# Performance work log

Hardware: AMD Instinct MI355X
Metric: run time of the kernel (lower is better)

Reference implementation:

```python
import jax, jax.numpy as jnp
import numpy as np
import math

NEG = -1e9
B, TX, TY, ODIM = 32, 512, 2048, 80


def setup_inputs() -> dict:
    key = jax.random.key(0)
    k1, k2 = jax.random.split(key)
    return {
        "x_m": jax.random.normal(k1, (B, TX, ODIM), jnp.float32),
        "x_logs": jnp.zeros((B, TX, ODIM), jnp.float32),  # mean_only=True -> zeros_like(x_m)
        "z": jax.random.normal(k2, (B, ODIM, TY), jnp.float32),
        "x_mask": jnp.ones((B, 1, TX), jnp.float32),
        "z_mask": jnp.ones((B, 1, TY), jnp.float32),
    }


def maximum_path(logp, mask, tx_len, ty_len):
    """Monotonic alignment search (Glow-TTS Viterbi DP).
    logp: [B, Tx, Ty] log-likelihoods; mask: [B, Tx, Ty]; lengths: [B] int32.
    Returns hard alignment path [B, Tx, Ty] in {0,1}.
    """
    B_, Tx, Ty = logp.shape
    xs = jnp.arange(Tx)
    logp = jnp.where(mask > 0, logp, NEG)

    # Forward DP over mel frames y: f[x,y] = logp[x,y] + max(f[x-1,y-1], f[x,y-1])
    def fwd_step(prev, y):
        v_cur = jnp.where(xs[None, :] == y, NEG, prev)              # stay (invalid on diagonal)
        prev_shift = jnp.concatenate(
            [jnp.full((B_, 1), NEG, logp.dtype), prev[:, :-1]], axis=1)
        v_prev = jnp.where(xs[None, :] == 0,
                           jnp.where(y == 0, jnp.zeros((), logp.dtype), jnp.asarray(NEG, logp.dtype)),
                           prev_shift)                               # advance
        f = logp[:, :, y] + jnp.maximum(v_prev, v_cur)
        return f, f

    _, fcols = jax.lax.scan(fwd_step, jnp.full((B_, Tx), NEG, logp.dtype), jnp.arange(Ty))
    # fcols: [Ty, B, Tx]

    # Backtrack from (tx_len-1, ty_len-1) down to y=0.
    def bwd_step(index, y):
        active = y < ty_len                                          # [B] bool
        row = jax.nn.one_hot(index, Tx, dtype=logp.dtype) * active[:, None].astype(logp.dtype)
        fm1 = fcols[jnp.maximum(y - 1, 0)]                           # [B, Tx]
        f_here = jnp.take_along_axis(fm1, index[:, None], axis=1)[:, 0]
        f_left = jnp.take_along_axis(fm1, jnp.maximum(index - 1, 0)[:, None], axis=1)[:, 0]
        move = (index != 0) & ((index == y) | (f_here < f_left))
        new_index = jnp.where(active & move, index - 1, index)
        return new_index, row

    _, rows = jax.lax.scan(bwd_step, tx_len - 1, jnp.arange(Ty - 1, -1, -1))
    path = jnp.flip(rows, axis=0).transpose(1, 2, 0)                 # [B, Tx, Ty]
    return path * mask


def reference(x_m, x_logs, z, x_mask, z_mask):
    # attn_mask: [B, Tx, Ty]
    attn_mask = x_mask[:, 0, :, None] * z_mask[:, 0, None, :]

    # Gaussian log-likelihood of each frame z[:, :, y] under each text token's N(x_m, exp(x_logs))
    x_s_sq_r = jnp.exp(-2.0 * x_logs)                                # [B, Tx, D]
    logp1 = jnp.sum(-0.5 * math.log(2.0 * math.pi) - x_logs, axis=2)[:, :, None]
    logp2 = jnp.einsum('btd,bdy->bty', x_s_sq_r, -0.5 * z * z)
    logp3 = jnp.einsum('btd,bdy->bty', x_m * x_s_sq_r, z)
    logp4 = jnp.sum(-0.5 * x_m * x_m * x_s_sq_r, axis=2)[:, :, None]
    logp = logp1 + logp2 + logp3 + logp4                             # [B, Tx, Ty]

    tx_len = jnp.sum(x_mask[:, 0, :], axis=1).astype(jnp.int32)
    ty_len = jnp.sum(z_mask[:, 0, :], axis=1).astype(jnp.int32)
    attn = jax.lax.stop_gradient(
        maximum_path(jax.lax.stop_gradient(logp), attn_mask, tx_len, ty_len))

    # Expand token stats to frame level with the hard alignment.
    z_m = jnp.einsum('bxy,bxd->bdy', attn, x_m)                      # [B, D, Ty]
    z_logs = jnp.einsum('bxy,bxd->bdy', attn, x_logs)                # [B, D, Ty]
    log_durations_ = jnp.log(1e-8 + jnp.sum(attn, axis=-1))[:, None, :] * x_mask  # [B, 1, Tx]
    return z_m, z_logs, log_durations_, attn
```

## Files before the change

kernel.cpp:

```cpp
#include <hip/hip_runtime.h>
#include <math.h>

#define B_ 32
#define TX_ 512
#define TY_ 2048
#define D_ 80
#define NEG (-1e9f)
#define PF 16

typedef float f32x4 __attribute__((ext_vector_type(4)));

__global__ __launch_bounds__(128) void prep_kernel(
    const float* __restrict__ x_m, const float* __restrict__ x_logs,
    float* __restrict__ Cc, int* __restrict__ flag)
{
    int row = blockIdx.x;
    int t = threadIdx.x;
    __shared__ float red[128];
    float contrib = 0.f;
    bool nz = false;
    if (t < D_) {
        float xl = x_logs[(size_t)row * D_ + t];
        float xm = x_m[(size_t)row * D_ + t];
        nz = (xl != 0.f);
        float a1 = expf(-2.f * xl);
        contrib = -0.91893853320467274178f - xl - 0.5f * xm * xm * a1;
    }
    unsigned long long m = __ballot(nz);
    if ((t & 63) == 0 && m) atomicOr(flag, 1);
    red[t] = contrib;
    __syncthreads();
    if (t < 64) {
        float v = red[t] + red[t + 64];
        #pragma unroll
        for (int off = 32; off >= 1; off >>= 1) v += __shfl_down(v, off);
        if (t == 0) Cc[row] = v;
    }
}

__global__ __launch_bounds__(256) void lens_kernel(const float* __restrict__ x_mask,
    const float* __restrict__ z_mask, int* __restrict__ lens)
{
    int blk = blockIdx.x; int t = threadIdx.x;
    __shared__ float red[256];
    float s = 0.f;
    if (blk < B_) {
        for (int i = t; i < TX_; i += 256) s += x_mask[(size_t)blk * TX_ + i];
    } else {
        int b = blk - B_;
        for (int i = t; i < TY_; i += 256) s += z_mask[(size_t)b * TY_ + i];
    }
    red[t] = s; __syncthreads();
    for (int off = 128; off >= 1; off >>= 1) {
        if (t < off) red[t] += red[t + off];
        __syncthreads();
    }
    if (t == 0) lens[blk] = (int)(red[0] + 0.5f);
}

__global__ __launch_bounds__(256) void gemm_zero(
    const int* __restrict__ flag,
    const float* __restrict__ x_m, const float* __restrict__ Cc,
    const float* __restrict__ z,
    const float* __restrict__ x_mask, const float* __restrict__ z_mask,
    float* __restrict__ logpT, int y0, int C)
{
    if (*flag != 0) return;
    __shared__ float xs[40][132];
    __shared__ float zs[40][132];
    int b = blockIdx.z;
    int x0 = blockIdx.x * 128;
    int cy0 = blockIdx.y * 128;
    int yy0 = y0 + cy0;
    int tid = threadIdx.x;
    int tm = tid & 15, tn = tid >> 4;
    float acc[8][8];
    float accz[8];
    #pragma unroll
    for (int i = 0; i < 8; ++i) {
        accz[i] = 0.f;
        #pragma unroll
        for (int j = 0; j < 8; ++j) acc[i][j] = 0.f;
    }

    for (int h = 0; h < 2; ++h) {
        if (h) __syncthreads();
        for (int i = tid; i < 128 * 40; i += 256) {
            int m = i / 40, d = i - m * 40;
            xs[d][m] = x_m[((size_t)(b * TX_ + x0 + m)) * D_ + h * 40 + d];
        }
        for (int i = tid; i < 40 * 128; i += 256) {
            int d = i >> 7, n = i & 127;
            zs[d][n] = z[((size_t)(b * D_ + h * 40 + d)) * TY_ + yy0 + n];
        }
        __syncthreads();
        #pragma unroll 4
        for (int k = 0; k < 40; ++k) {
            f32x4 a0 = *(const f32x4*)&xs[k][tm * 4];
            f32x4 a1 = *(const f32x4*)&xs[k][64 + tm * 4];
            f32x4 z0 = *(const f32x4*)&zs[k][tn * 4];
            f32x4 z1 = *(const f32x4*)&zs[k][64 + tn * 4];
            float av[8], zv[8];
            #pragma unroll
            for (int i = 0; i < 4; ++i) { av[i] = a0[i]; av[i+4] = a1[i]; zv[i] = z0[i]; zv[i+4] = z1[i]; }
            #pragma unroll
            for (int j = 0; j < 8; ++j) {
                accz[j] = fmaf(zv[j], zv[j], accz[j]);
                #pragma unroll
                for (int i = 0; i < 8; ++i)
                    acc[i][j] = fmaf(av[i], zv[j], acc[i][j]);
            }
        }
    }
    f32x4 ccA = *(const f32x4*)&Cc[(size_t)b * TX_ + x0 + tm * 4];
    f32x4 ccB = *(const f32x4*)&Cc[(size_t)b * TX_ + x0 + 64 + tm * 4];
    f32x4 xmA = *(const f32x4*)&x_mask[(size_t)b * TX_ + x0 + tm * 4];
    f32x4 xmB = *(const f32x4*)&x_mask[(size_t)b * TX_ + x0 + 64 + tm * 4];
    #pragma unroll
    for (int jj = 0; jj < 8; ++jj) {
        int n = (jj < 4) ? (tn * 4 + jj) : (64 + tn * 4 + (jj - 4));
        float zmv = z_mask[(size_t)b * TY_ + yy0 + n];
        float sz = -0.5f * accz[jj];
        f32x4 oA, oB;
        #pragma unroll
        for (int i = 0; i < 4; ++i) {
            float vA = acc[i][jj] + ccA[i] + sz;
            float vB = acc[i + 4][jj] + ccB[i] + sz;
            oA[i] = (xmA[i] * zmv > 0.f) ? vA : NEG;
            oB[i] = (xmB[i] * zmv > 0.f) ? vB : NEG;
        }
        float* orow = &logpT[((size_t)b * C + cy0 + n) * TX_ + x0];
        *(f32x4*)(orow + tm * 4) = oA;
        *(f32x4*)(orow + 64 + tm * 4) = oB;
    }
}

__global__ __launch_bounds__(256) void gemm_logp(
    const int* __restrict__ flag,
    const float* __restrict__ x_m, const float* __restrict__ x_logs,
    const float* __restrict__ Cc,
    const float* __restrict__ z, const float* __restrict__ x_mask, const float* __restrict__ z_mask,
    float* __restrict__ logpT, int y0, int C)
{
    if (*flag == 0) return;
    __shared__ float A1s[D_][72];
    __shared__ float A2s[D_][72];
    __shared__ float zs[D_][64];
    int b = blockIdx.z;
    int x0 = blockIdx.x * 64;
    int cy0 = blockIdx.y * 64;
    int yy0 = y0 + cy0;
    int tid = threadIdx.x;
    for (int i = tid; i < 64 * D_; i += 256) {
        int m = i / D_, d = i - m * D_;
        size_t ga = ((size_t)(b * TX_ + x0 + m)) * D_ + d;
        float xl = x_logs[ga], xm = x_m[ga];
        float a1 = expf(-2.f * xl);
        A1s[d][m] = a1;
        A2s[d][m] = xm * a1;
    }
    for (int i = tid; i < D_ * 64; i += 256) {
        int d = i >> 6, n = i & 63;
        zs[d][n] = z[((size_t)(b * D_ + d)) * TY_ + yy0 + n];
    }
    __syncthreads();
    int tm = tid & 15, tn = tid >> 4;
    float acc[4][4];
    #pragma unroll
    for (int i = 0; i < 4; ++i)
        #pragma unroll
        for (int j = 0; j < 4; ++j) acc[i][j] = 0.f;
    #pragma unroll 4
    for (int k = 0; k < D_; ++k) {
        f32x4 a1 = *(const f32x4*)&A1s[k][tm * 4];
        f32x4 a2 = *(const f32x4*)&A2s[k][tm * 4];
        f32x4 zv = *(const f32x4*)&zs[k][tn * 4];
        #pragma unroll
        for (int j = 0; j < 4; ++j) {
            float h = -0.5f * zv[j];
            #pragma unroll
            for (int i = 0; i < 4; ++i) {
                float tt = fmaf(h, a1[i], a2[i]);
                acc[i][j] = fmaf(zv[j], tt, acc[i][j]);
            }
        }
    }
    f32x4 cc = *(const f32x4*)&Cc[(size_t)b * TX_ + x0 + tm * 4];
    f32x4 xm = *(const f32x4*)&x_mask[(size_t)b * TX_ + x0 + tm * 4];
    #pragma unroll
    for (int j = 0; j < 4; ++j) {
        int n = tn * 4 + j;
        float zmv = z_mask[(size_t)b * TY_ + yy0 + n];
        f32x4 o;
        #pragma unroll
        for (int i = 0; i < 4; ++i) {
            float val = acc[i][j] + cc[i];
            o[i] = (xm[i] * zmv > 0.f) ? val : NEG;
        }
        *(f32x4*)&logpT[((size_t)b * C + cy0 + n) * TX_ + x0 + tm * 4] = o;
    }
}

__device__ __forceinline__ void dp_stepN(int lane, const float4 la, const float4 lb,
    float (&f)[8], unsigned int laneMask, unsigned char* bpp)
{
    float lp8[8] = {la.x, la.y, la.z, la.w, lb.x, lb.y, lb.z, lb.w};
    float sh = __shfl_up(f[7], 1);
    float pm0 = (lane == 0) ? NEG : sh;
    unsigned int byt = 0u;
    #pragma unroll
    for (int j = 7; j >= 0; --j) {
        float pm = (j == 0) ? pm0 : f[j - 1];
        byt = byt * 2u + ((f[j] < pm) ? 1u : 0u);
        f[j] = lp8[j] + fmaxf(pm, f[j]);
    }
    *bpp = (unsigned char)(byt & laneMask);
}

__device__ __forceinline__ void dp_stepD(int y, int lane, const float4 la, const float4 lb,
    float (&f)[8], unsigned int laneMask, unsigned char* bpp)
{
    float lp8[8] = {la.x, la.y, la.z, la.w, lb.x, lb.y, lb.z, lb.w};
    float sh = __shfl_up(f[7], 1);
    float edge = (y == 0) ? 0.f : NEG;
    float pm0 = (lane == 0) ? edge : sh;
    bool lanehit = (lane == (y >> 3));
    int jeq = y & 7;
    unsigned int byt = 0u;
    #pragma unroll
    for (int j = 7; j >= 0; --j) {
        float pm = (j == 0) ? pm0 : f[j - 1];
        bool ceq = lanehit && (jeq == j);
        byt = byt * 2u + (((f[j] < pm) || ceq) ? 1u : 0u);
        float vc = ceq ? NEG : f[j];
        f[j] = lp8[j] + fmaxf(pm, vc);
    }
    *bpp = (unsigned char)(byt & laneMask);
}

__global__ __launch_bounds__(64, 1) void dp_forward(const float* __restrict__ logpT,
    float* __restrict__ fsave, unsigned char* __restrict__ bits8, int y0, int C)
{
    int b = blockIdx.x, lane = threadIdx.x;
    const float* lp = logpT + (size_t)b * C * TX_ + lane * 8;
    unsigned char* bp = bits8 + ((size_t)b * TY_ + y0) * 64 + lane;
    float f[8];
    if (y0 == 0) {
        #pragma unroll
        for (int j = 0; j < 8; ++j) f[j] = NEG;
    } else {
        float4 fa = *(const float4*)(fsave + (size_t)b * TX_ + lane * 8);
        float4 fb = *(const float4*)(fsave + (size_t)b * TX_ + lane * 8 + 4);
        f[0]=fa.x; f[1]=fa.y; f[2]=fa.z; f[3]=fa.w;
        f[4]=fb.x; f[5]=fb.y; f[6]=fb.z; f[7]=fb.w;
    }
    unsigned int laneMask = (lane == 0) ? 0xFEu : 0xFFu;

    float4 bufA[PF], bufB[PF];
    #pragma unroll
    for (int s = 0; s < PF; ++s) {
        bufA[s] = *(const float4*)(lp + (size_t)s * TX_);
        bufB[s] = *(const float4*)(lp + (size_t)s * TX_ + 4);
    }
    int tD = 0;
    if (y0 < TX_) { tD = TX_ - y0; if (tD > C) tD = C; }
    int t = 0;
    for (; t < tD; t += PF) {
        #pragma unroll
        for (int s = 0; s < PF; ++s) {
            dp_stepD(y0 + t + s, lane, bufA[s], bufB[s], f, laneMask, bp + (size_t)(t + s) * 64);
            int tn = t + s + PF; if (tn >= C) tn = C - 1;
            bufA[s] = *(const float4*)(lp + (size_t)tn * TX_);
            bufB[s] = *(const float4*)(lp + (size_t)tn * TX_ + 4);
        }
    }
    for (; t < C; t += PF) {
        #pragma unroll
        for (int s = 0; s < PF; ++s) {
            dp_stepN(lane, bufA[s], bufB[s], f, laneMask, bp + (size_t)(t + s) * 64);
            int tn = t + s + PF; if (tn >= C) tn = C - 1;
            bufA[s] = *(const float4*)(lp + (size_t)tn * TX_);
            bufB[s] = *(const float4*)(lp + (size_t)tn * TX_ + 4);
        }
    }
    float4 fa = make_float4(f[0], f[1], f[2], f[3]);
    float4 fb = make_float4(f[4], f[5], f[6], f[7]);
    *(float4*)(fsave + (size_t)b * TX_ + lane * 8) = fa;
    *(float4*)(fsave + (size_t)b * TX_ + lane * 8 + 4) = fb;
}

__global__ __launch_bounds__(64) void backtrack_kernel(
    const unsigned char* __restrict__ bits8, const int* __restrict__ lens,
    const float* __restrict__ x_mask, int* __restrict__ idxA, float* __restrict__ logdur)
{
    int b = blockIdx.x, lane = threadIdx.x;
    __shared__ int durS[TX_];
    for (int x = lane; x < TX_; x += 64) durS[x] = 0;
    int tx_len = lens[b];
    int ty_len = lens[B_ + b];
    int idx = tx_len - 1;
    if (idx < 0) idx = 0;
    int cnt = 0;
    const unsigned long long* bu = (const unsigned long long*)(bits8 + (size_t)b * TY_ * 64);
    for (int w = 0; w < TY_ / 64; ++w) {
        int ytop = TY_ - 1 - w * 64;
        int yl = ytop - lane;
        int Whi = idx >> 6;
        unsigned long long whi = bu[(size_t)yl * 8 + Whi];
        unsigned long long wlo = (Whi > 0) ? bu[(size_t)yl * 8 + Whi - 1] : 0ull;
        int rec = -1;
        for (int s = 0; s < 64; ++s) {
            int y = ytop - s;
            bool active = (y < ty_len);
            if (lane == s) rec = active ? idx : -1;
            if (active) cnt++;
            unsigned long long wsel = ((idx >> 6) == Whi) ? __shfl(whi, s) : __shfl(wlo, s);
            int bit = (int)((wsel >> (idx & 63)) & 1ull);
            if (active && bit) {
                if (lane == 0) durS[idx] = cnt;
                cnt = 0;
                idx -= 1;
            }
        }
        idxA[(size_t)b * TY_ + yl] = rec;
    }
    if (lane == 0) durS[idx] = cnt;
    __syncthreads();
    for (int x = lane; x < TX_; x += 64) {
        float dv = (float)durS[x];
        logdur[(size_t)b * TX_ + x] = logf(1e-8f + dv) * x_mask[(size_t)b * TX_ + x];
    }
}

__global__ __launch_bounds__(256) void attn_write(const int* __restrict__ idxA,
    const float* __restrict__ x_mask, const float* __restrict__ z_mask,
    float* __restrict__ attn_o)
{
    int b = blockIdx.z; int x = blockIdx.y;
    int yq = blockIdx.x * 256 + threadIdx.x;
    int4 iv = ((const int4*)(idxA + (size_t)b * TY_))[yq];
    float xm = x_mask[(size_t)b * TX_ + x];
    float4 zm4 = ((const float4*)(z_mask + (size_t)b * TY_))[yq];
    float4 o;
    o.x = (iv.x == x) ? xm * zm4.x : 0.f;
    o.y = (iv.y == x) ? xm * zm4.y : 0.f;
    o.z = (iv.z == x) ? xm * zm4.z : 0.f;
    o.w = (iv.w == x) ? xm * zm4.w : 0.f;
    ((float4*)(attn_o + ((size_t)(b * TX_ + x)) * TY_))[yq] = o;
}

__global__ __launch_bounds__(256) void zm_write(const int* __restrict__ idxA,
    const float* __restrict__ x_m, const float* __restrict__ x_logs,
    const float* __restrict__ x_mask, const float* __restrict__ z_mask,
    float* __restrict__ z_m_o, float* __restrict__ z_logs_o)
{
    int b = blockIdx.z; int d = blockIdx.y;
    int yq = blockIdx.x * 256 + threadIdx.x;
    int4 iv = ((const int4*)(idxA + (size_t)b * TY_))[yq];
    float4 zm4 = ((const float4*)(z_mask + (size_t)b * TY_))[yq];
    float4 om, ol;
    float* omv = (float*)&om; float* olv = (float*)&ol;
    int ivv[4] = {iv.x, iv.y, iv.z, iv.w};
    float zmv[4] = {zm4.x, zm4.y, zm4.z, zm4.w};
    #pragma unroll
    for (int c = 0; c < 4; ++c) {
        float vm = 0.f, vl = 0.f;
        int ix = ivv[c];
        if (ix >= 0) {
            float wgt = x_mask[(size_t)b * TX_ + ix] * zmv[c];
            size_t ga = ((size_t)(b * TX_ + ix)) * D_ + d;
            vm = wgt * x_m[ga];
            vl = wgt * x_logs[ga];
        }
        omv[c] = vm; olv[c] = vl;
    }
    ((float4*)(z_m_o    + ((size_t)(b * D_ + d)) * TY_))[yq] = om;
    ((float4*)(z_logs_o + ((size_t)(b * D_ + d)) * TY_))[yq] = ol;
}

extern "C" void kernel_launch(void* const* d_in, const int* in_sizes, int n_in,
                              void* d_out, int out_size, void* d_ws, size_t ws_size,
                              hipStream_t stream)
{
    const float* x_m    = (const float*)d_in[0];
    const float* x_logs = (const float*)d_in[1];
    const float* z      = (const float*)d_in[2];
    const float* x_mask = (const float*)d_in[3];
    const float* z_mask = (const float*)d_in[4];
    float* out = (float*)d_out;
    float* z_m_o    = out;
    float* z_logs_o = out + (size_t)B_ * D_ * TY_;
    float* logdur_o = out + (size_t)2 * B_ * D_ * TY_;
    float* attn_o   = logdur_o + (size_t)B_ * TX_;

    char* p = (char*)d_ws;
    float* Cc = (float*)p;            p += (size_t)B_ * TX_ * 4;
    float* fs = (float*)p;            p += (size_t)B_ * TX_ * 4;
    unsigned char* bits8 = (unsigned char*)p; p += (size_t)B_ * TY_ * 64;
    int* idxA = (int*)p;              p += (size_t)B_ * TY_ * 4;
    int* lens = (int*)p;              p += 256;
    int* flag = (int*)p;              p += 256;
    float* logpC = (float*)p;
    size_t fixed = (size_t)(p - (char*)d_ws);
    size_t avail = (ws_size > fixed) ? (ws_size - fixed) : 0;
    int C = 128;
    const int cands[5] = {2048, 1024, 512, 256, 128};
    for (int i = 0; i < 5; ++i) {
        if ((size_t)B_ * cands[i] * TX_ * 4 <= avail) { C = cands[i]; break; }
    }

    hipMemsetAsync(flag, 0, sizeof(int), stream);
    prep_kernel<<<B_ * TX_, 128, 0, stream>>>(x_m, x_logs, Cc, flag);
    lens_kernel<<<2 * B_, 256, 0, stream>>>(x_mask, z_mask, lens);
    int nc = TY_ / C;
    for (int c = 0; c < nc; ++c) {
        gemm_zero<<<dim3(TX_ / 128, C / 128, B_), 256, 0, stream>>>(
            flag, x_m, Cc, z, x_mask, z_mask, logpC, c * C, C);
        gemm_logp<<<dim3(TX_ / 64, C / 64, B_), 256, 0, stream>>>(
            flag, x_m, x_logs, Cc, z, x_mask, z_mask, logpC, c * C, C);
        dp_forward<<<B_, 64, 0, stream>>>(logpC, fs, bits8, c * C, C);
    }
    backtrack_kernel<<<B_, 64, 0, stream>>>(bits8, lens, x_mask, idxA, logdur_o);
    attn_write<<<dim3(TY_ / 4 / 256, TX_, B_), 256, 0, stream>>>(idxA, x_mask, z_mask, attn_o);
    zm_write<<<dim3(TY_ / 4 / 256, D_, B_), 256, 0, stream>>>(
        idxA, x_m, x_logs, x_mask, z_mask, z_m_o, z_logs_o);
}
```

Baseline: 652.0 us.

## Parallelize forward DP across 8 wavefronts with redundant shadow recompute for cross-wave dependencies

Result: slower. 728.0 us (+11.7%).

```diff
diff --git a/kernel.cpp b/kernel.cpp
--- a/kernel.cpp
+++ b/kernel.cpp
@@ -7,6 +7,8 @@
 #define D_ 80
 #define NEG (-1e9f)
 #define PF 16
+#define DPW 8
+#define EP 64
 
 typedef float f32x4 __attribute__((ext_vector_type(4)));
 
@@ -201,92 +203,73 @@
     }
 }
 
-__device__ __forceinline__ void dp_stepN(int lane, const float4 la, const float4 lb,
-    float (&f)[8], unsigned int laneMask, unsigned char* bpp)
-{
-    float lp8[8] = {la.x, la.y, la.z, la.w, lb.x, lb.y, lb.z, lb.w};
-    float sh = __shfl_up(f[7], 1);
-    float pm0 = (lane == 0) ? NEG : sh;
-    unsigned int byt = 0u;
-    #pragma unroll
-    for (int j = 7; j >= 0; --j) {
-        float pm = (j == 0) ? pm0 : f[j - 1];
-        byt = byt * 2u + ((f[j] < pm) ? 1u : 0u);
-        f[j] = lp8[j] + fmaxf(pm, f[j]);
-    }
-    *bpp = (unsigned char)(byt & laneMask);
-}
-
-__device__ __forceinline__ void dp_stepD(int y, int lane, const float4 la, const float4 lb,
-    float (&f)[8], unsigned int laneMask, unsigned char* bpp)
-{
-    float lp8[8] = {la.x, la.y, la.z, la.w, lb.x, lb.y, lb.z, lb.w};
-    float sh = __shfl_up(f[7], 1);
-    float edge = (y == 0) ? 0.f : NEG;
-    float pm0 = (lane == 0) ? edge : sh;
-    bool lanehit = (lane == (y >> 3));
-    int jeq = y & 7;
-    unsigned int byt = 0u;
-    #pragma unroll
-    for (int j = 7; j >= 0; --j) {
-        float pm = (j == 0) ? pm0 : f[j - 1];
-        bool ceq = lanehit && (jeq == j);
-        byt = byt * 2u + (((f[j] < pm) || ceq) ? 1u : 0u);
-        float vc = ceq ? NEG : f[j];
-        f[j] = lp8[j] + fmaxf(pm, vc);
-    }
-    *bpp = (unsigned char)(byt & laneMask);
-}
-
-__global__ __launch_bounds__(64, 1) void dp_forward(const float* __restrict__ logpT,
+__global__ __launch_bounds__(512, 1) void dp_forward(const float* __restrict__ logpT,
     float* __restrict__ fsave, unsigned char* __restrict__ bits8, int y0, int C)
 {
-    int b = blockIdx.x, lane = threadIdx.x;
-    const float* lp = logpT + (size_t)b * C * TX_ + lane * 8;
-    unsigned char* bp = bits8 + ((size_t)b * TY_ + y0) * 64 + lane;
-    float f[8];
-    if (y0 == 0) {
-        #pragma unroll
-        for (int j = 0; j < 8; ++j) f[j] = NEG;
-    } else {
-        float4 fa = *(const float4*)(fsave + (size_t)b * TX_ + lane * 8);
-        float4 fb = *(const float4*)(fsave + (size_t)b * TX_ + lane * 8 + 4);
-        f[0]=fa.x; f[1]=fa.y; f[2]=fa.z; f[3]=fa.w;
-        f[4]=fb.x; f[5]=fb.y; f[6]=fb.z; f[7]=fb.w;
-    }
-    unsigned int laneMask = (lane == 0) ? 0xFEu : 0xFFu;
-
-    float4 bufA[PF], bufB[PF];
+    int b = blockIdx.x, tid = threadIdx.x;
+    int w = tid >> 6, lane = tid & 63;
+    __shared__ float fpubS[512];
+    __shared__ unsigned long long bitsS[EP * DPW];
+    const float* lpP = logpT + (size_t)b * C * TX_ + tid;
+    const float* lpS = logpT + (size_t)b * C * TX_ + (tid >= 64 ? tid - 64 : tid);
+    int xsh = tid - 64;
+
+    float f;
+    if (y0 == 0) f = NEG;
+    else f = fsave[(size_t)b * TX_ + tid];
+    fpubS[tid] = f;
+    __syncthreads();
+    float fsh = (w == 0) ? NEG : fpubS[tid - 64];
+    __syncthreads();
+
+    float ringP[PF], ringS[PF];
     #pragma unroll
     for (int s = 0; s < PF; ++s) {
-        bufA[s] = *(const float4*)(lp + (size_t)s * TX_);
-        bufB[s] = *(const float4*)(lp + (size_t)s * TX_ + 4);
-    }
-    int tD = 0;
-    if (y0 < TX_) { tD = TX_ - y0; if (tD > C) tD = C; }
-    int t = 0;
-    for (; t < tD; t += PF) {
-        #pragma unroll
-        for (int s = 0; s < PF; ++s) {
-            dp_stepD(y0 + t + s, lane, bufA[s], bufB[s], f, laneMask, bp + (size_t)(t + s) * 64);
-            int tn = t + s + PF; if (tn >= C) tn = C - 1;
-            bufA[s] = *(const float4*)(lp + (size_t)tn * TX_);
-            bufB[s] = *(const float4*)(lp + (size_t)tn * TX_ + 4);
-        }
-    }
-    for (; t < C; t += PF) {
-        #pragma unroll
-        for (int s = 0; s < PF; ++s) {
-            dp_stepN(lane, bufA[s], bufB[s], f, laneMask, bp + (size_t)(t + s) * 64);
-            int tn = t + s + PF; if (tn >= C) tn = C - 1;
-            bufA[s] = *(const float4*)(lp + (size_t)tn * TX_);
-            bufB[s] = *(const float4*)(lp + (size_t)tn * TX_ + 4);
-        }
-    }
-    float4 fa = make_float4(f[0], f[1], f[2], f[3]);
-    float4 fb = make_float4(f[4], f[5], f[6], f[7]);
-    *(float4*)(fsave + (size_t)b * TX_ + lane * 8) = fa;
-    *(float4*)(fsave + (size_t)b * TX_ + lane * 8 + 4) = fb;
+        ringP[s] = lpP[(size_t)s * TX_];
+        ringS[s] = lpS[(size_t)s * TX_];
+    }
+    unsigned long long keep0 = (w == 0) ? ~1ull : ~0ull;
+
+    for (int t0 = 0; t0 < C; t0 += EP) {
+        for (int tt = 0; tt < EP; tt += PF) {
+            #pragma unroll
+            for (int s = 0; s < PF; ++s) {
+                int t = t0 + tt + s;
+                int y = y0 + t;
+                float lpv = ringP[s];
+                float lsv = ringS[s];
+                int tn = t + PF; if (tn >= C) tn = C - 1;
+                ringP[s] = lpP[(size_t)tn * TX_];
+                ringS[s] = lpS[(size_t)tn * TX_];
+                float fO = f, fshO = fsh;
+                float upP = __shfl_up(fO, 1);
+                float upS = __shfl_up(fshO, 1);
+                float b63 = __shfl(fshO, 63);
+                float edge = (y == 0) ? 0.f : NEG;
+                float pmP = (lane == 0) ? ((w == 0) ? edge : b63) : upP;
+                bool ceqP = (y == tid);
+                bool predP = (fO < pmP) || ceqP;
+                unsigned long long word = __ballot(predP);
+                float vcP = ceqP ? NEG : fO;
+                f = lpv + fmaxf(pmP, vcP);
+                float pmS = (lane == 0) ? ((xsh == 0) ? edge : NEG) : upS;
+                bool ceqS = (y == xsh);
+                float vcS = ceqS ? NEG : fshO;
+                fsh = lsv + fmaxf(pmS, vcS);
+                if (lane == 0) bitsS[(t & (EP - 1)) * DPW + w] = word & keep0;
+            }
+        }
+        fpubS[tid] = f;
+        __syncthreads();
+        {
+            unsigned long long wv = bitsS[tid];
+            int k = tid >> 3, ww = tid & 7;
+            *(unsigned long long*)(bits8 + ((size_t)b * TY_ + y0 + t0 + k) * 64 + ww * 8) = wv;
+        }
+        fsh = (w == 0) ? NEG : fpubS[tid - 64];
+        __syncthreads();
+    }
+    fsave[(size_t)b * TX_ + tid] = f;
 }
 
 __global__ __launch_bounds__(64) void backtrack_kernel(
@@ -418,7 +401,7 @@
             flag, x_m, Cc, z, x_mask, z_mask, logpC, c * C, C);
         gemm_logp<<<dim3(TX_ / 64, C / 64, B_), 256, 0, stream>>>(
             flag, x_m, x_logs, Cc, z, x_mask, z_mask, logpC, c * C, C);
-        dp_forward<<<B_, 64, 0, stream>>>(logpC, fs, bits8, c * C, C);
+        dp_forward<<<B_, 512, 0, stream>>>(logpC, fs, bits8, c * C, C);
     }
     backtrack_kernel<<<B_, 64, 0, stream>>>(bits8, lens, x_mask, idxA, logdur_o);
     attn_write<<<dim3(TY_ / 4 / 256, TX_, B_), 256, 0, stream>>>(idxA, x_mask, z_mask, attn_o);
```

## Stream DP logp rows into an LDS ring via async global_load_lds

Applied to the files above, without the earlier changes.

New measurement: 1.079 ms. +65.5%, slower.

```diff
diff --git a/kernel.cpp b/kernel.cpp
--- a/kernel.cpp
+++ b/kernel.cpp
@@ -6,9 +6,12 @@
 #define TY_ 2048
 #define D_ 80
 #define NEG (-1e9f)
-#define PF 16
+#define NS 16
 
 typedef float f32x4 __attribute__((ext_vector_type(4)));
+
+#define GLB(p) ((const __attribute__((address_space(1))) void*)(p))
+#define LDSP(p) ((__attribute__((address_space(3))) void*)(p))
 
 __global__ __launch_bounds__(128) void prep_kernel(
     const float* __restrict__ x_m, const float* __restrict__ x_logs,
@@ -201,26 +204,12 @@
     }
 }
 
-__device__ __forceinline__ void dp_stepN(int lane, const float4 la, const float4 lb,
-    float (&f)[8], unsigned int laneMask, unsigned char* bpp)
-{
-    float lp8[8] = {la.x, la.y, la.z, la.w, lb.x, lb.y, lb.z, lb.w};
-    float sh = __shfl_up(f[7], 1);
-    float pm0 = (lane == 0) ? NEG : sh;
-    unsigned int byt = 0u;
-    #pragma unroll
-    for (int j = 7; j >= 0; --j) {
-        float pm = (j == 0) ? pm0 : f[j - 1];
-        byt = byt * 2u + ((f[j] < pm) ? 1u : 0u);
-        f[j] = lp8[j] + fmaxf(pm, f[j]);
-    }
-    *bpp = (unsigned char)(byt & laneMask);
-}
-
-__device__ __forceinline__ void dp_stepD(int y, int lane, const float4 la, const float4 lb,
-    float (&f)[8], unsigned int laneMask, unsigned char* bpp)
-{
-    float lp8[8] = {la.x, la.y, la.z, la.w, lb.x, lb.y, lb.z, lb.w};
+__device__ __forceinline__ unsigned int dp_step(int y, int lane, const f32x4 la, const f32x4 lb,
+    float (&f)[8], unsigned int laneMask)
+{
+    float lp8[8];
+    #pragma unroll
+    for (int i = 0; i < 4; ++i) { lp8[i] = la[i]; lp8[i + 4] = lb[i]; }
     float sh = __shfl_up(f[7], 1);
     float edge = (y == 0) ? 0.f : NEG;
     float pm0 = (lane == 0) ? edge : sh;
@@ -235,58 +224,61 @@
         float vc = ceq ? NEG : f[j];
         f[j] = lp8[j] + fmaxf(pm, vc);
     }
-    *bpp = (unsigned char)(byt & laneMask);
+    return byt & laneMask;
 }
 
 __global__ __launch_bounds__(64, 1) void dp_forward(const float* __restrict__ logpT,
     float* __restrict__ fsave, unsigned char* __restrict__ bits8, int y0, int C)
 {
+    __shared__ float ring[NS][TX_];
+    __shared__ float trash[TX_];
     int b = blockIdx.x, lane = threadIdx.x;
-    const float* lp = logpT + (size_t)b * C * TX_ + lane * 8;
+    const char* rowbase = (const char*)(logpT + (size_t)b * C * TX_) + lane * 16;
     unsigned char* bp = bits8 + ((size_t)b * TY_ + y0) * 64 + lane;
     float f[8];
     if (y0 == 0) {
         #pragma unroll
         for (int j = 0; j < 8; ++j) f[j] = NEG;
     } else {
-        float4 fa = *(const float4*)(fsave + (size_t)b * TX_ + lane * 8);
-        float4 fb = *(const float4*)(fsave + (size_t)b * TX_ + lane * 8 + 4);
-        f[0]=fa.x; f[1]=fa.y; f[2]=fa.z; f[3]=fa.w;
-        f[4]=fb.x; f[5]=fb.y; f[6]=fb.z; f[7]=fb.w;
+        f32x4 fa = *(const f32x4*)(fsave + (size_t)b * TX_ + lane * 8);
+        f32x4 fb = *(const f32x4*)(fsave + (size_t)b * TX_ + lane * 8 + 4);
+        #pragma unroll
+        for (int j = 0; j < 4; ++j) { f[j] = fa[j]; f[j + 4] = fb[j]; }
     }
     unsigned int laneMask = (lane == 0) ? 0xFEu : 0xFFu;
 
-    float4 bufA[PF], bufB[PF];
-    #pragma unroll
-    for (int s = 0; s < PF; ++s) {
-        bufA[s] = *(const float4*)(lp + (size_t)s * TX_);
-        bufB[s] = *(const float4*)(lp + (size_t)s * TX_ + 4);
-    }
-    int tD = 0;
-    if (y0 < TX_) { tD = TX_ - y0; if (tD > C) tD = C; }
-    int t = 0;
-    for (; t < tD; t += PF) {
-        #pragma unroll
-        for (int s = 0; s < PF; ++s) {
-            dp_stepD(y0 + t + s, lane, bufA[s], bufB[s], f, laneMask, bp + (size_t)(t + s) * 64);
-            int tn = t + s + PF; if (tn >= C) tn = C - 1;
-            bufA[s] = *(const float4*)(lp + (size_t)tn * TX_);
-            bufB[s] = *(const float4*)(lp + (size_t)tn * TX_ + 4);
-        }
-    }
-    for (; t < C; t += PF) {
-        #pragma unroll
-        for (int s = 0; s < PF; ++s) {
-            dp_stepN(lane, bufA[s], bufB[s], f, laneMask, bp + (size_t)(t + s) * 64);
-            int tn = t + s + PF; if (tn >= C) tn = C - 1;
-            bufA[s] = *(const float4*)(lp + (size_t)tn * TX_);
-            bufB[s] = *(const float4*)(lp + (size_t)tn * TX_ + 4);
-        }
-    }
-    float4 fa = make_float4(f[0], f[1], f[2], f[3]);
-    float4 fb = make_float4(f[4], f[5], f[6], f[7]);
-    *(float4*)(fsave + (size_t)b * TX_ + lane * 8) = fa;
-    *(float4*)(fsave + (size_t)b * TX_ + lane * 8 + 4) = fb;
+    #pragma unroll
+    for (int s = 0; s < NS; ++s) {
+        const char* g = rowbase + (size_t)s * (TX_ * 4);
+        __builtin_amdgcn_global_load_lds(GLB(g),        LDSP(&ring[s][0]),   16, 0, 0);
+        __builtin_amdgcn_global_load_lds(GLB(g + 1024), LDSP(&ring[s][256]), 16, 0, 0);
+    }
+
+    for (int t = 0; t < C; ++t) {
+        asm volatile("s_waitcnt vmcnt(30)" ::: "memory");
+        __builtin_amdgcn_sched_barrier(0);
+        int slot = t & (NS - 1);
+        f32x4 la = *(const f32x4*)&ring[slot][lane * 8];
+        f32x4 lb = *(const f32x4*)&ring[slot][lane * 8 + 4];
+        unsigned int byt = dp_step(y0 + t, lane, la, lb, f, laneMask);
+        bp[(size_t)t * 64] = (unsigned char)byt;
+        asm volatile("s_waitcnt lgkmcnt(0)" ::: "memory");
+        __builtin_amdgcn_sched_barrier(0);
+        int tn = t + NS;
+        if (tn < C) {
+            const char* g = rowbase + (size_t)tn * (TX_ * 4);
+            __builtin_amdgcn_global_load_lds(GLB(g),        LDSP(&ring[slot][0]),   16, 0, 0);
+            __builtin_amdgcn_global_load_lds(GLB(g + 1024), LDSP(&ring[slot][256]), 16, 0, 0);
+        } else {
+            __builtin_amdgcn_global_load_lds(GLB(rowbase),        LDSP(&trash[0]),   16, 0, 0);
+            __builtin_amdgcn_global_load_lds(GLB(rowbase + 1024), LDSP(&trash[256]), 16, 0, 0);
+        }
+    }
+    f32x4 fa, fb;
+    #pragma unroll
+    for (int j = 0; j < 4; ++j) { fa[j] = f[j]; fb[j] = f[j + 4]; }
+    *(f32x4*)(fsave + (size_t)b * TX_ + lane * 8) = fa;
+    *(f32x4*)(fsave + (size_t)b * TX_ + lane * 8 + 4) = fb;
 }
 
 __global__ __launch_bounds__(64) void backtrack_kernel(
```
